# Kernel optimization log

Measured on AMD Instinct MI355X. Metric: run time of the kernel, lower is better.

## Reference

```python
import jax, jax.numpy as jnp
import numpy as np

EPS = 1e-5
HEADS, DK, DV = 8, 32, 32


def conv3x3(x, w, b):
    # regular (non-depthwise, despite the name) 3x3 conv, stride 1, padding 1
    y = jax.lax.conv_general_dilated(
        x, w, window_strides=(1, 1), padding='SAME',
        dimension_numbers=('NCHW', 'OIHW', 'NCHW'))
    return y + b[None, :, None, None]


def setup_inputs() -> dict:
    key = jax.random.key(0)
    ks = jax.random.split(key, 16)
    C = 256
    d = {}
    d['x'] = jax.random.normal(ks[0], (8, C, 32, 32), jnp.float32)
    s_lin = 1.0 / np.sqrt(C)
    s_conv = 1.0 / np.sqrt(C * 9)
    d['Wq'] = jax.random.normal(ks[1], (C, HEADS * DK), jnp.float32) * s_lin
    d['bq'] = jnp.zeros((HEADS * DK,), jnp.float32)
    d['conv_k_w'] = jax.random.normal(ks[2], (C, C, 3, 3), jnp.float32) * s_conv
    d['conv_k_b'] = jnp.zeros((C,), jnp.float32)
    d['Wk'] = jax.random.normal(ks[3], (C, HEADS * DK), jnp.float32) * s_lin
    d['bk'] = jnp.zeros((HEADS * DK,), jnp.float32)
    d['conv_v_w'] = jax.random.normal(ks[4], (C, C, 3, 3), jnp.float32) * s_conv
    d['conv_v_b'] = jnp.zeros((C,), jnp.float32)
    d['Wv'] = jax.random.normal(ks[5], (C, HEADS * DV), jnp.float32) * s_lin
    d['bv'] = jnp.zeros((HEADS * DV,), jnp.float32)
    d['Wo'] = jax.random.normal(ks[6], (HEADS * DV, C), jnp.float32) * s_lin
    d['bo'] = jnp.zeros((C,), jnp.float32)
    d['B'] = jax.random.normal(ks[7], (1, HEADS, 1024, 1024), jnp.float32) * 0.02
    return d


def reference(x, Wq, bq, conv_k_w, conv_k_b, Wk, bk, conv_v_w, conv_v_b, Wv, bv, Wo, bo, B):
    b, c, h, w = x.shape
    hw = h * w
    xr = x.reshape(b, c, hw).transpose(0, 2, 1)  # [b, hw, c]
    # F.layer_norm with normalized_shape == full shape: whole-tensor stats, no affine
    m = jnp.mean(xr)
    v = jnp.mean((xr - m) ** 2)
    xn = (xr - m) * jax.lax.rsqrt(v + EPS)

    q = (xn @ Wq + bq).reshape(b, hw, HEADS, DK).transpose(0, 2, 1, 3)  # [b,H,hw,dk]

    k = conv3x3(x, conv_k_w, conv_k_b)  # stride 1 -> same spatial size (per source)
    k = k.reshape(b, c, hw).transpose(0, 2, 1)
    k = (k @ Wk + bk).reshape(b, hw, HEADS, DK).transpose(0, 2, 1, 3)

    vv = conv3x3(x, conv_v_w, conv_v_b)
    vv = vv.reshape(b, c, hw).transpose(0, 2, 1)
    vv = (vv @ Wv + bv).reshape(b, hw, HEADS, DV).transpose(0, 2, 1, 3)

    scale = DK ** (-0.5)
    attn = jnp.einsum('bhid,bhjd->bhij', q, k) * scale + B  # [b,H,hw,hw]
    attn = jax.nn.softmax(attn, axis=-1)
    out = jnp.einsum('bhij,bhjd->bhid', attn, vv)  # [b,H,hw,dv]
    out = out.transpose(0, 2, 1, 3).reshape(b, hw, HEADS * DV)
    out = out @ Wo + bo  # [b, hw, c]
    # faithful to torch .view(b, c, h, w): raw reshape, NO transpose
    out = out.reshape(b, c, h, w)
    return out + x
```

## Files before the change

kernel.cpp:

```cpp
#include <hip/hip_runtime.h>
#include <hip/hip_bf16.h>
#include <math.h>

#define B_     8
#define C_     256
#define HW_    1024
#define NTOT   (B_*C_*HW_)
#define HEADS_ 8
#define DK_    32
#define SCALE_ 0.17677669529663687f

#define F_STATS 0
#define F_PART  16
#define F_YK2   8192
#define F_YV2   (F_YK2 + NTOT)
#define F_XB    (F_YV2 + NTOT)
#define F_WT    (F_XB + NTOT/2)
#define F_QB    (F_WT + 589824)
#define F_KB    (F_QB + NTOT/2)
#define F_VT    (F_KB + NTOT/2)

typedef float f32x4 __attribute__((ext_vector_type(4)));
typedef short short8 __attribute__((ext_vector_type(8)));

__device__ __forceinline__ short bf16s(float f) {
    __hip_bfloat16 h = __float2bfloat16(f);
    return *(short*)&h;
}
__device__ __forceinline__ unsigned pack_bf16(float a, float b) {
    unsigned ua = (unsigned short)bf16s(a);
    unsigned ub = (unsigned short)bf16s(b);
    return ua | (ub << 16);
}
__device__ __forceinline__ void gload_lds16(const short* g, short* l) {
    __builtin_amdgcn_global_load_lds(
        (const __attribute__((address_space(1))) unsigned*)g,
        (__attribute__((address_space(3))) unsigned*)l, 16, 0, 0);
}

__global__ void k_prep_x(const float* __restrict__ x, short* __restrict__ xb,
                         float* __restrict__ part) {
    __shared__ short t[64 * 258];
    __shared__ float ls[4], ls2[4];
    int b = blockIdx.x >> 4, p0 = (blockIdx.x & 15) << 6;
    int tid = threadIdx.x;
    float s = 0.f, s2 = 0.f;
    for (int i = tid; i < 256 * 64; i += 256) {
        int ci = i >> 6, p = i & 63;
        float v = x[(b * C_ + ci) * HW_ + p0 + p];
        s += v; s2 += v * v;
        t[p * 258 + ci] = bf16s(v);
    }
    for (int o = 32; o; o >>= 1) { s += __shfl_down(s, o); s2 += __shfl_down(s2, o); }
    int wid = tid >> 6, lane = tid & 63;
    if (lane == 0) { ls[wid] = s; ls2[wid] = s2; }
    __syncthreads();
    if (tid == 0) {
        float a = 0.f, bb = 0.f;
        for (int i = 0; i < 4; i++) { a += ls[i]; bb += ls2[i]; }
        part[blockIdx.x * 2] = a; part[blockIdx.x * 2 + 1] = bb;
    }
    for (int i = tid; i < 64 * 256; i += 256) {
        int p = i >> 8, ci = i & 255;
        xb[(b * HW_ + p0 + p) * C_ + ci] = t[p * 258 + ci];
    }
}

__global__ void k_stats(const float* __restrict__ part, float* __restrict__ stats) {
    __shared__ float ls[256], ls2[256];
    float s = 0.f, s2 = 0.f;
    for (int i = threadIdx.x; i < 128; i += 256) { s += part[2 * i]; s2 += part[2 * i + 1]; }
    ls[threadIdx.x] = s; ls2[threadIdx.x] = s2;
    __syncthreads();
    for (int off = 128; off; off >>= 1) {
        if (threadIdx.x < off) { ls[threadIdx.x] += ls[threadIdx.x + off]; ls2[threadIdx.x] += ls2[threadIdx.x + off]; }
        __syncthreads();
    }
    if (threadIdx.x == 0) {
        float m = ls[0] / (float)NTOT;
        float var = ls2[0] / (float)NTOT - m * m;
        stats[0] = m;
        stats[1] = rsqrtf(var + 1e-5f);
    }
}

__global__ void k_prep_w(const float* __restrict__ wk, const float* __restrict__ wv,
                         short* __restrict__ wt) {
    int idx = blockIdx.x * 256 + threadIdx.x;
    int ci0 = (idx << 2) & 255;
    int rest = idx >> 6;
    int n = rest & 511, tap = rest >> 9;
    const float* src = (n < 256) ? (wk + (n * C_) * 9) : (wv + ((n - 256) * C_) * 9);
    short4 o;
    short* op = (short*)&o;
    for (int u = 0; u < 4; u++)
        op[u] = bf16s(src[(ci0 + u) * 9 + tap]);
    *(short4*)&wt[((tap * 512 + n) * C_) + ci0] = o;
}

__global__ void k_prep_pw(const float* __restrict__ Wq, const float* __restrict__ Wk,
                          const float* __restrict__ Wv, const float* __restrict__ Wo,
                          short* __restrict__ wt4) {
    __shared__ short t[64 * 66];
    int mi = blockIdx.x >> 4, tl = blockIdx.x & 15;
    int c0 = (tl >> 2) * 64, e0 = (tl & 3) * 64;
    const float* W = mi == 0 ? Wq : mi == 1 ? Wk : mi == 2 ? Wv : Wo;
    int tid = threadIdx.x;
    for (int i = tid; i < 4096; i += 256) {
        int cl = i >> 6, el = i & 63;
        t[cl * 66 + el] = bf16s(W[(c0 + cl) * 256 + e0 + el]);
    }
    __syncthreads();
    for (int i = tid; i < 4096; i += 256) {
        int el = i >> 6, cl = i & 63;
        wt4[mi * 65536 + (e0 + el) * 256 + c0 + cl] = t[cl * 66 + el];
    }
}

__global__ void k_prep_beta(const float* __restrict__ Wq, const float* __restrict__ bq,
                            const float* __restrict__ stats, float* __restrict__ beta0) {
    __shared__ float ps[1024];
    int t = threadIdx.x, e = t & 255, part = t >> 8;
    float s = 0.f;
    for (int c = part * 64; c < part * 64 + 64; c++) s += Wq[c * 256 + e];
    ps[t] = s;
    __syncthreads();
    if (t < 256) {
        float cs = ps[t] + ps[t + 256] + ps[t + 512] + ps[t + 768];
        beta0[t] = (bq[t] - stats[0] * stats[1] * cs) * SCALE_;
    }
}

__device__ __forceinline__ int a_off(int slot, int chunk) {
    int c = chunk ^ (slot & 3);
    int s = slot ^ ((slot >> 2) & 1);
    return s * 64 + c * 16;
}

__global__ __launch_bounds__(512, 4)
void k_conv_mfma(const short* __restrict__ xb, const short* __restrict__ wt,
                 const float* __restrict__ bk, const float* __restrict__ bv,
                 float* __restrict__ yk2, float* __restrict__ yv2) {
    __shared__ short a_sh[204 * 32];
    __shared__ short b_sh[9 * 2048];
    int bid = blockIdx.x;
    int nt = bid & 7, pt = (bid >> 3) & 7, b = bid >> 6;
    int R0 = pt * 4;
    int tid = threadIdx.x;
    int w = tid >> 6, l = tid & 63;
    int wm = w >> 1, wn = w & 1;
    int col16 = l & 15, kq = l >> 4;

    int offs[2], loffs[2];
    #pragma unroll
    for (int it = 0; it < 2; it++) {
        int i = tid + it * 512;
        if (i < 816) {
            int slot = i >> 2, chunk = i & 3;
            int ty = slot / 34, tx = slot - ty * 34;
            int Y = R0 - 1 + ty, X = tx - 1;
            offs[it] = ((unsigned)Y < 32u && (unsigned)X < 32u)
                       ? ((b * HW_ + Y * 32 + X) * C_ + chunk * 8) : -1;
            loffs[it] = a_off(slot, chunk);
        } else { offs[it] = -1; loffs[it] = -1; }
    }

    int bgoff[5];
    int nbj = 0;
    #pragma unroll 1
    for (int j = w; j < 36; j += 8) {
        int S = j * 64 + l;
        int tap = S >> 8, s = S & 255;
        int colb = s >> 2, kqs = s & 3;
        int kq2 = kqs ^ ((colb >> 1) & 3);
        bgoff[nbj++] = (tap * 512 + nt * 64 + colb) * C_ + kq2 * 8;
    }

    f32x4 acc[2][2];
    #pragma unroll
    for (int m = 0; m < 2; m++)
        #pragma unroll
        for (int n = 0; n < 2; n++) acc[m][n] = (f32x4)0.f;

    int sr[2];
    #pragma unroll
    for (int nf = 0; nf < 2; nf++) {
        int colb = wn * 32 + nf * 16 + col16;
        sr[nf] = (colb << 2) | (kq ^ ((colb >> 1) & 3));
    }

    {
        short8 sv[2];
        #pragma unroll
        for (int it = 0; it < 2; it++)
            sv[it] = (offs[it] >= 0) ? *(const short8*)(xb + offs[it]) : (short8)0;
        int jj = 0;
        #pragma unroll 1
        for (int j = w; j < 36; j += 8, jj++)
            gload_lds16(wt + bgoff[jj], b_sh + j * 512);
        #pragma unroll
        for (int it = 0; it < 2; it++)
            if (loffs[it] >= 0) *(short8*)((char*)a_sh + loffs[it]) = sv[it];
    }
    __syncthreads();

    #pragma unroll 1
    for (int step = 0; step < 8; step++) {
        const char* ab = (const char*)a_sh;
        const char* bbp = (const char*)b_sh;
        #pragma unroll
        for (int tap = 0; tap < 9; tap++) {
            const int dyi = tap / 3, dxi = tap % 3;
            short8 af[2], bf[2];
            #pragma unroll
            for (int mf = 0; mf < 2; mf++) {
                int slot = (wm + dyi) * 34 + mf * 16 + col16 + dxi;
                af[mf] = *(const short8*)(ab + a_off(slot, kq));
            }
            #pragma unroll
            for (int nf = 0; nf < 2; nf++)
                bf[nf] = *(const short8*)(bbp + tap * 4096 + sr[nf] * 16);
            #pragma unroll
            for (int mf = 0; mf < 2; mf++)
                #pragma unroll
                for (int nf = 0; nf < 2; nf++)
                    acc[mf][nf] = __builtin_amdgcn_mfma_f32_16x16x32_bf16(af[mf], bf[nf], acc[mf][nf], 0, 0, 0);
        }
        if (step < 7) {
            int ci0n = step * 32 + 32;
            __syncthreads();
            short8 sv[2];
            #pragma unroll
            for (int it = 0; it < 2; it++)
                sv[it] = (offs[it] >= 0) ? *(const short8*)(xb + offs[it] + ci0n) : (short8)0;
            int jj = 0;
            #pragma unroll 1
            for (int j = w; j < 36; j += 8, jj++)
                gload_lds16(wt + bgoff[jj] + ci0n, b_sh + j * 512);
            #pragma unroll
            for (int it = 0; it < 2; it++)
                if (loffs[it] >= 0) *(short8*)((char*)a_sh + loffs[it]) = sv[it];
            __syncthreads();
        }
    }

    const bool isv = (nt >= 4);
    float* dst = isv ? yv2 : yk2;
    const float* bias = isv ? bv : bk;
    int cbase = (nt & 3) * 64 + wn * 32 + col16;
    #pragma unroll
    for (int nf = 0; nf < 2; nf++) {
        int co = cbase + nf * 16;
        float bi = bias[co];
        #pragma unroll
        for (int mf = 0; mf < 2; mf++) {
            #pragma unroll
            for (int r = 0; r < 4; r++) {
                int pixel = pt * 128 + wm * 32 + mf * 16 + kq * 4 + r;
                dst[(b * HW_ + pixel) * C_ + co] = acc[mf][nf][r] + bi;
            }
        }
    }
}

__global__ void k_proj_mfma(const short* __restrict__ xb,
                            const float* __restrict__ yk2, const float* __restrict__ yv2,
                            const short* __restrict__ wt4,
                            const float* __restrict__ bkp, const float* __restrict__ bvp,
                            const float* __restrict__ stats, const float* __restrict__ beta0,
                            short* __restrict__ qb, short* __restrict__ kb,
                            short* __restrict__ vt) {
    __shared__ char smem[17408];
    int pj = blockIdx.x, pt = blockIdx.y, b = blockIdx.z;
    int p0 = pt * 32;
    int tid = threadIdx.x, w = tid >> 6, l = tid & 63;
    int c16 = l & 15, kq = l >> 4;

    if (pj == 0) {
        #pragma unroll
        for (int it = 0; it < 4; it++) {
            int i = it * 256 + tid;
            int slab = i >> 7, rem = i & 127, slot = rem >> 2, chunk = rem & 3;
            short8 v = *(const short8*)(xb + ((b * HW_ + p0 + slot) * C_ + slab * 32 + chunk * 8));
            *(short8*)(smem + slab * 2048 + a_off(slot, chunk)) = v;
        }
    } else {
        const float* src = (pj == 1) ? yk2 : yv2;
        #pragma unroll
        for (int it = 0; it < 4; it++) {
            int i = it * 256 + tid;
            int slab = i >> 7, rem = i & 127, slot = rem >> 2, chunk = rem & 3;
            const float* sp = src + (b * HW_ + p0 + slot) * C_ + slab * 32 + chunk * 8;
            float4 f0 = *(const float4*)sp;
            float4 f1 = *(const float4*)(sp + 4);
            short8 v;
            v[0] = bf16s(f0.x); v[1] = bf16s(f0.y); v[2] = bf16s(f0.z); v[3] = bf16s(f0.w);
            v[4] = bf16s(f1.x); v[5] = bf16s(f1.y); v[6] = bf16s(f1.z); v[7] = bf16s(f1.w);
            *(short8*)(smem + slab * 2048 + a_off(slot, chunk)) = v;
        }
    }
    __syncthreads();

    const short* wt_p = wt4 + pj * 65536;
    f32x4 acc[2][4];
    #pragma unroll
    for (int m = 0; m < 2; m++)
        #pragma unroll
        for (int n = 0; n < 4; n++) acc[m][n] = (f32x4)0.f;

    for (int s = 0; s < 8; s++) {
        short8 af[2], bf[4];
        #pragma unroll
        for (int mf = 0; mf < 2; mf++)
            af[mf] = *(const short8*)(smem + s * 2048 + a_off(mf * 16 + c16, kq));
        #pragma unroll
        for (int nf = 0; nf < 4; nf++)
            bf[nf] = *(const short8*)(wt_p + (w * 64 + nf * 16 + c16) * 256 + s * 32 + kq * 8);
        #pragma unroll
        for (int mf = 0; mf < 2; mf++)
            #pragma unroll
            for (int nf = 0; nf < 4; nf++)
                acc[mf][nf] = __builtin_amdgcn_mfma_f32_16x16x32_bf16(af[mf], bf[nf], acc[mf][nf], 0, 0, 0);
    }

    float alpha = (pj == 0) ? stats[1] * SCALE_ : 1.f;
    float beta[4];
    #pragma unroll
    for (int nf = 0; nf < 4; nf++) {
        int e = w * 64 + nf * 16 + c16;
        beta[nf] = (pj == 0) ? beta0[e] : (pj == 1 ? bkp[e] : bvp[e]);
    }
    __syncthreads();

    short* rp = (short*)smem + w * 2176;
    if (pj < 2) {
        #pragma unroll
        for (int mf = 0; mf < 2; mf++)
            #pragma unroll
            for (int nf = 0; nf < 4; nf++)
                #pragma unroll
                for (int rg = 0; rg < 4; rg++) {
                    int px = mf * 16 + kq * 4 + rg, el = nf * 16 + c16;
                    rp[px * 66 + el] = bf16s(alpha * acc[mf][nf][rg] + beta[nf]);
                }
        __syncthreads();
        short* dst = (pj == 0) ? qb : kb;
        #pragma unroll
        for (int j = 0; j < 4; j++) {
            int px = j * 8 + (l >> 3), el = (l & 7) * 8;
            short8 v = *(const short8*)(rp + px * 66 + el);
            int e = w * 64 + el, h = e >> 5, d = e & 31;
            *(short8*)(dst + ((b * 8 + h) * HW_ + p0 + px) * DK_ + d) = v;
        }
    } else {
        #pragma unroll
        for (int mf = 0; mf < 2; mf++)
            #pragma unroll
            for (int nf = 0; nf < 4; nf++)
                #pragma unroll
                for (int rg = 0; rg < 4; rg++) {
                    int px = mf * 16 + kq * 4 + rg, el = nf * 16 + c16;
                    rp[el * 34 + px] = bf16s(acc[mf][nf][rg] + beta[nf]);
                }
        __syncthreads();
        #pragma unroll
        for (int j = 0; j < 4; j++) {
            int el = j * 16 + (l >> 2), px = (l & 3) * 8;
            short8 v = *(const short8*)(rp + el * 34 + px);
            int e = w * 64 + el, h = e >> 5, d = e & 31;
            *(short8*)(vt + ((b * 8 + h) * DK_ + d) * HW_ + p0 + px) = v;
        }
    }
}

__global__ __launch_bounds__(256, 4)
void k_attn(const short* __restrict__ qb, const short* __restrict__ kb,
            const short* __restrict__ vt, const float* __restrict__ Bb,
            short* __restrict__ ao) {
    __shared__ __align__(16) short Ks[128 * 32];
    __shared__ __align__(16) short Vs[32 * 128];
    int bid = blockIdx.x;
    int h = bid & 7, b = (bid >> 3) & 7, qt = bid >> 6;
    int bh = b * HEADS_ + h;
    int tid = threadIdx.x, w = tid >> 6, l = tid & 63;
    int g = l >> 4, c16 = l & 15;

    int qrow = qt * 64 + w * 16 + c16;
    short8 qf = *(const short8*)(qb + (bh * HW_ + qrow) * DK_ + g * 8);
    const float* Brow = Bb + (h * HW_ + qrow) * HW_;

    float4 breg[8];
    #pragma unroll
    for (int mt = 0; mt < 8; mt++)
        breg[mt] = *(const float4*)(Brow + mt * 16 + g * 4);

    float m_run = -1e30f, l_run = 0.f;
    f32x4 ot[2];
    ot[0] = (f32x4)0.f; ot[1] = (f32x4)0.f;

    int vrow = tid >> 4, vch = tid & 15;
    int vrow2 = (tid + 256) >> 4, vch2 = (tid + 256) & 15;
    const short* kbase = kb + bh * HW_ * DK_;

    for (int kv0 = 0; kv0 < HW_; kv0 += 128) {
        __syncthreads();
        gload_lds16(kbase + kv0 * DK_ + (w * 2) * 512 + l * 8, Ks + (w * 2) * 512);
        gload_lds16(kbase + kv0 * DK_ + (w * 2 + 1) * 512 + l * 8, Ks + (w * 2 + 1) * 512);
        {
            short8 v0 = *(const short8*)(vt + (bh * DK_ + vrow) * HW_ + kv0 + vch * 8);
            short8 v1 = *(const short8*)(vt + (bh * DK_ + vrow2) * HW_ + kv0 + vch2 * 8);
            *(short8*)((char*)Vs + vrow * 256 + ((vch * 16) ^ ((vrow & 7) << 4))) = v0;
            *(short8*)((char*)Vs + vrow2 * 256 + ((vch2 * 16) ^ ((vrow2 & 7) << 4))) = v1;
        }
        __syncthreads();

        f32x4 st[8];
        __builtin_amdgcn_s_setprio(1);
        #pragma unroll
        for (int mt = 0; mt < 8; mt++) {
            f32x4 acc;
            acc[0] = breg[mt].x; acc[1] = breg[mt].y; acc[2] = breg[mt].z; acc[3] = breg[mt].w;
            short8 kf = *(const short8*)(Ks + (mt * 16 + c16) * DK_ + g * 8);
            st[mt] = __builtin_amdgcn_mfma_f32_16x16x32_bf16(kf, qf, acc, 0, 0, 0);
        }
        __builtin_amdgcn_s_setprio(0);
        if (kv0 + 128 < HW_) {
            #pragma unroll
            for (int mt = 0; mt < 8; mt++)
                breg[mt] = *(const float4*)(Brow + kv0 + 128 + mt * 16 + g * 4);
        }

        float pmax = st[0][0];
        #pragma unroll
        for (int mt = 0; mt < 8; mt++)
            #pragma unroll
            for (int rg = 0; rg < 4; rg++) pmax = fmaxf(pmax, st[mt][rg]);
        pmax = fmaxf(pmax, __shfl_xor(pmax, 16));
        pmax = fmaxf(pmax, __shfl_xor(pmax, 32));
        if (!__all(pmax <= m_run + 8.f)) {
            float mnew = fmaxf(m_run, pmax);
            float f = __expf(m_run - mnew);
            m_run = mnew;
            l_run *= f;
            int fv = __float_as_int(f);
            #pragma unroll
            for (int rg = 0; rg < 4; rg++) {
                float fr = __int_as_float(__builtin_amdgcn_ds_bpermute((g * 4 + rg) << 2, fv));
                ot[0][rg] *= fr;
                ot[1][rg] *= fr;
            }
        }
        float s = 0.f;
        #pragma unroll
        for (int mt = 0; mt < 8; mt++)
            #pragma unroll
            for (int rg = 0; rg < 4; rg++) {
                float e_ = __expf(st[mt][rg] - m_run);
                st[mt][rg] = e_;
                s += e_;
            }
        s += __shfl_xor(s, 16);
        s += __shfl_xor(s, 32);
        l_run += s;

        short8 pa[4];
        #pragma unroll
        for (int kt = 0; kt < 4; kt++) {
            unsigned u0 = pack_bf16(st[2 * kt][0], st[2 * kt][1]);
            unsigned u1 = pack_bf16(st[2 * kt][2], st[2 * kt][3]);
            unsigned u2 = pack_bf16(st[2 * kt + 1][0], st[2 * kt + 1][1]);
            unsigned u3 = pack_bf16(st[2 * kt + 1][2], st[2 * kt + 1][3]);
            unsigned* pu = (unsigned*)&pa[kt];
            pu[0] = u0; pu[1] = u1; pu[2] = u2; pu[3] = u3;
        }

        __builtin_amdgcn_s_setprio(1);
        #pragma unroll
        for (int kt = 0; kt < 4; kt++) {
            #pragma unroll
            for (int nt = 0; nt < 2; nt++) {
                int dv = c16 + 16 * nt;
                int X0 = kt * 64 + 8 * g;
                int X1 = X0 + 32;
                int a0 = dv * 256 + ((((X0 >> 4) ^ (dv & 7)) << 4) | (X0 & 15));
                int a1 = dv * 256 + ((((X1 >> 4) ^ (dv & 7)) << 4) | (X1 & 15));
                unsigned long long lo = *(const unsigned long long*)((char*)Vs + a0);
                unsigned long long hi = *(const unsigned long long*)((char*)Vs + a1);
                short8 vf;
                *(unsigned long long*)&vf = lo;
                *((unsigned long long*)&vf + 1) = hi;
                ot[nt] = __builtin_amdgcn_mfma_f32_16x16x32_bf16(pa[kt], vf, ot[nt], 0, 0, 0);
            }
        }
        __builtin_amdgcn_s_setprio(0);
    }

    float linv = 1.f / l_run;
    int lrv = __float_as_int(linv);
    #pragma unroll
    for (int rg = 0; rg < 4; rg++) {
        float li = __int_as_float(__builtin_amdgcn_ds_bpermute((g * 4 + rg) << 2, lrv));
        int qg = qt * 64 + w * 16 + g * 4 + rg;
        #pragma unroll
        for (int nt = 0; nt < 2; nt++)
            ao[(b * HW_ + qg) * C_ + h * DK_ + nt * 16 + c16] = bf16s(ot[nt][rg] * li);
    }
}

__global__ void k_out_mfma(const short* __restrict__ aob, const short* __restrict__ wot,
                           const float* __restrict__ bo, const float* __restrict__ x,
                           float* __restrict__ out) {
    __shared__ char smem[16384];
    int pt = blockIdx.x, b = blockIdx.y;
    int p0 = pt * 32;
    int tid = threadIdx.x, w = tid >> 6, l = tid & 63;
    int c16 = l & 15, kq = l >> 4;

    #pragma unroll
    for (int it = 0; it < 4; it++) {
        int i = it * 256 + tid;
        int slab = i >> 7, rem = i & 127, slot = rem >> 2, chunk = rem & 3;
        short8 v = *(const short8*)(aob + ((b * HW_ + p0 + slot) * C_ + slab * 32 + chunk * 8));
        *(short8*)(smem + slab * 2048 + a_off(slot, chunk)) = v;
    }
    __syncthreads();

    f32x4 acc[2][4];
    #pragma unroll
    for (int m = 0; m < 2; m++)
        #pragma unroll
        for (int n = 0; n < 4; n++) acc[m][n] = (f32x4)0.f;

    for (int s = 0; s < 8; s++) {
        short8 af[2], bf[4];
        #pragma unroll
        for (int mf = 0; mf < 2; mf++)
            af[mf] = *(const short8*)(smem + s * 2048 + a_off(mf * 16 + c16, kq));
        #pragma unroll
        for (int nf = 0; nf < 4; nf++)
            bf[nf] = *(const short8*)(wot + (w * 64 + nf * 16 + c16) * 256 + s * 32 + kq * 8);
        #pragma unroll
        for (int mf = 0; mf < 2; mf++)
            #pragma unroll
            for (int nf = 0; nf < 4; nf++)
                acc[mf][nf] = __builtin_amdgcn_mfma_f32_16x16x32_bf16(af[mf], bf[nf], acc[mf][nf], 0, 0, 0);
    }

    #pragma unroll
    for (int nf = 0; nf < 4; nf++) {
        int e = w * 64 + nf * 16 + c16;
        float bov = bo[e];
        #pragma unroll
        for (int mf = 0; mf < 2; mf++) {
            #pragma unroll
            for (int rg = 0; rg < 4; rg++) {
                int px = mf * 16 + kq * 4 + rg;
                int idx = b * (C_ * HW_) + (p0 + px) * 256 + e;
                out[idx] = acc[mf][nf][rg] + bov + x[idx];
            }
        }
    }
}

extern "C" void kernel_launch(void* const* d_in, const int* in_sizes, int n_in,
                              void* d_out, int out_size, void* d_ws, size_t ws_size,
                              hipStream_t stream) {
    const float* x   = (const float*)d_in[0];
    const float* Wq  = (const float*)d_in[1];
    const float* bq  = (const float*)d_in[2];
    const float* ckw = (const float*)d_in[3];
    const float* ckb = (const float*)d_in[4];
    const float* Wk  = (const float*)d_in[5];
    const float* bk  = (const float*)d_in[6];
    const float* cvw = (const float*)d_in[7];
    const float* cvb = (const float*)d_in[8];
    const float* Wv  = (const float*)d_in[9];
    const float* bv  = (const float*)d_in[10];
    const float* Wo  = (const float*)d_in[11];
    const float* bo  = (const float*)d_in[12];
    const float* Bb  = (const float*)d_in[13];
    float* ws  = (float*)d_ws;
    float* out = (float*)d_out;

    short* xb      = (short*)(ws + F_XB);
    short* wt      = (short*)(ws + F_WT);
    short* wt4     = (short*)(ws + F_WT);
    float* beta0   = ws + F_WT + 131072;
    short* qb      = (short*)(ws + F_QB);
    short* kb      = (short*)(ws + F_KB);
    short* vt      = (short*)(ws + F_VT);
    short* aob     = (short*)(ws + F_YK2);
    short* wot     = wt4 + 3 * 65536;

    k_prep_x   <<<128,  256, 0, stream>>>(x, xb, ws + F_PART);
    k_stats    <<<1,    256, 0, stream>>>(ws + F_PART, ws + F_STATS);
    k_prep_w   <<<1152, 256, 0, stream>>>(ckw, cvw, wt);
    k_conv_mfma<<<512,  512, 0, stream>>>(xb, wt, ckb, cvb, ws + F_YK2, ws + F_YV2);
    k_prep_pw  <<<64,   256, 0, stream>>>(Wq, Wk, Wv, Wo, wt4);
    k_prep_beta<<<1,   1024, 0, stream>>>(Wq, bq, ws + F_STATS, beta0);
    k_proj_mfma<<<dim3(3, 32, 8), 256, 0, stream>>>(xb, ws + F_YK2, ws + F_YV2,
                                                    wt4, bk, bv, ws + F_STATS, beta0,
                                                    qb, kb, vt);
    k_attn     <<<1024, 256, 0, stream>>>(qb, kb, vt, Bb, aob);
    k_out_mfma <<<dim3(32, 8), 256, 0, stream>>>(aob, wot, bo, x, out);
}
```

Measured before the change: 143.1 us.

## Split attention over key halves, store conv outputs in bf16, widen prep_x grid

The attention kernel is split-K over two key halves. Each block writes unnormalized partial outputs plus running max and sum, and a new combine kernel merges them, which doubles the grid from 1024 to 2048 blocks and raises the occupancy hint. The conv kernel now writes its K/V activations as bf16 instead of fp32, so the projection kernel loads bf16 directly and moves half the bytes. k_prep_x uses 256 smaller blocks for more parallelism. The cost is an extra kernel launch and a round trip of the partial results through memory, plus an extra bf16 rounding of the partial outputs.

After: 220.6 us. 1.54x slower.

```diff
diff --git a/kernel.cpp b/kernel.cpp
--- a/kernel.cpp
+++ b/kernel.cpp
@@ -27,6 +27,10 @@
     __hip_bfloat16 h = __float2bfloat16(f);
     return *(short*)&h;
 }
+__device__ __forceinline__ float bf2f(short s) {
+    unsigned u = ((unsigned)(unsigned short)s) << 16;
+    return __int_as_float((int)u);
+}
 __device__ __forceinline__ unsigned pack_bf16(float a, float b) {
     unsigned ua = (unsigned short)bf16s(a);
     unsigned ub = (unsigned short)bf16s(b);
@@ -40,13 +44,13 @@
 
 __global__ void k_prep_x(const float* __restrict__ x, short* __restrict__ xb,
                          float* __restrict__ part) {
-    __shared__ short t[64 * 258];
+    __shared__ short t[32 * 258];
     __shared__ float ls[4], ls2[4];
-    int b = blockIdx.x >> 4, p0 = (blockIdx.x & 15) << 6;
+    int b = blockIdx.x >> 5, p0 = (blockIdx.x & 31) << 5;
     int tid = threadIdx.x;
     float s = 0.f, s2 = 0.f;
-    for (int i = tid; i < 256 * 64; i += 256) {
-        int ci = i >> 6, p = i & 63;
+    for (int i = tid; i < 256 * 32; i += 256) {
+        int ci = i >> 5, p = i & 31;
         float v = x[(b * C_ + ci) * HW_ + p0 + p];
         s += v; s2 += v * v;
         t[p * 258 + ci] = bf16s(v);
@@ -60,7 +64,7 @@
         for (int i = 0; i < 4; i++) { a += ls[i]; bb += ls2[i]; }
         part[blockIdx.x * 2] = a; part[blockIdx.x * 2 + 1] = bb;
     }
-    for (int i = tid; i < 64 * 256; i += 256) {
+    for (int i = tid; i < 32 * 256; i += 256) {
         int p = i >> 8, ci = i & 255;
         xb[(b * HW_ + p0 + p) * C_ + ci] = t[p * 258 + ci];
     }
@@ -68,8 +72,7 @@
 
 __global__ void k_stats(const float* __restrict__ part, float* __restrict__ stats) {
     __shared__ float ls[256], ls2[256];
-    float s = 0.f, s2 = 0.f;
-    for (int i = threadIdx.x; i < 128; i += 256) { s += part[2 * i]; s2 += part[2 * i + 1]; }
+    float s = part[2 * threadIdx.x], s2 = part[2 * threadIdx.x + 1];
     ls[threadIdx.x] = s; ls2[threadIdx.x] = s2;
     __syncthreads();
     for (int off = 128; off; off >>= 1) {
@@ -140,7 +143,7 @@
 __global__ __launch_bounds__(512, 4)
 void k_conv_mfma(const short* __restrict__ xb, const short* __restrict__ wt,
                  const float* __restrict__ bk, const float* __restrict__ bv,
-                 float* __restrict__ yk2, float* __restrict__ yv2) {
+                 short* __restrict__ yk2b, short* __restrict__ yv2b) {
     __shared__ short a_sh[204 * 32];
     __shared__ short b_sh[9 * 2048];
     int bid = blockIdx.x;
@@ -245,7 +248,7 @@
     }
 
     const bool isv = (nt >= 4);
-    float* dst = isv ? yv2 : yk2;
+    short* dst = isv ? yv2b : yk2b;
     const float* bias = isv ? bv : bk;
     int cbase = (nt & 3) * 64 + wn * 32 + col16;
     #pragma unroll
@@ -257,14 +260,14 @@
             #pragma unroll
             for (int r = 0; r < 4; r++) {
                 int pixel = pt * 128 + wm * 32 + mf * 16 + kq * 4 + r;
-                dst[(b * HW_ + pixel) * C_ + co] = acc[mf][nf][r] + bi;
+                dst[(b * HW_ + pixel) * C_ + co] = bf16s(acc[mf][nf][r] + bi);
             }
         }
     }
 }
 
 __global__ void k_proj_mfma(const short* __restrict__ xb,
-                            const float* __restrict__ yk2, const float* __restrict__ yv2,
+                            const short* __restrict__ yk2b, const short* __restrict__ yv2b,
                             const short* __restrict__ wt4,
                             const float* __restrict__ bkp, const float* __restrict__ bvp,
                             const float* __restrict__ stats, const float* __restrict__ beta0,
@@ -276,28 +279,13 @@
     int tid = threadIdx.x, w = tid >> 6, l = tid & 63;
     int c16 = l & 15, kq = l >> 4;
 
-    if (pj == 0) {
-        #pragma unroll
-        for (int it = 0; it < 4; it++) {
-            int i = it * 256 + tid;
-            int slab = i >> 7, rem = i & 127, slot = rem >> 2, chunk = rem & 3;
-            short8 v = *(const short8*)(xb + ((b * HW_ + p0 + slot) * C_ + slab * 32 + chunk * 8));
-            *(short8*)(smem + slab * 2048 + a_off(slot, chunk)) = v;
-        }
-    } else {
-        const float* src = (pj == 1) ? yk2 : yv2;
-        #pragma unroll
-        for (int it = 0; it < 4; it++) {
-            int i = it * 256 + tid;
-            int slab = i >> 7, rem = i & 127, slot = rem >> 2, chunk = rem & 3;
-            const float* sp = src + (b * HW_ + p0 + slot) * C_ + slab * 32 + chunk * 8;
-            float4 f0 = *(const float4*)sp;
-            float4 f1 = *(const float4*)(sp + 4);
-            short8 v;
-            v[0] = bf16s(f0.x); v[1] = bf16s(f0.y); v[2] = bf16s(f0.z); v[3] = bf16s(f0.w);
-            v[4] = bf16s(f1.x); v[5] = bf16s(f1.y); v[6] = bf16s(f1.z); v[7] = bf16s(f1.w);
-            *(short8*)(smem + slab * 2048 + a_off(slot, chunk)) = v;
-        }
+    const short* src = pj == 0 ? xb : (pj == 1 ? yk2b : yv2b);
+    #pragma unroll
+    for (int it = 0; it < 4; it++) {
+        int i = it * 256 + tid;
+        int slab = i >> 7, rem = i & 127, slot = rem >> 2, chunk = rem & 3;
+        short8 v = *(const short8*)(src + ((b * HW_ + p0 + slot) * C_ + slab * 32 + chunk * 8));
+        *(short8*)(smem + slab * 2048 + a_off(slot, chunk)) = v;
     }
     __syncthreads();
 
@@ -373,14 +361,14 @@
     }
 }
 
-__global__ __launch_bounds__(256, 4)
+__global__ __launch_bounds__(256, 8)
 void k_attn(const short* __restrict__ qb, const short* __restrict__ kb,
             const short* __restrict__ vt, const float* __restrict__ Bb,
-            short* __restrict__ ao) {
+            short* __restrict__ pob, float* __restrict__ pml) {
     __shared__ __align__(16) short Ks[128 * 32];
     __shared__ __align__(16) short Vs[32 * 128];
     int bid = blockIdx.x;
-    int h = bid & 7, b = (bid >> 3) & 7, qt = bid >> 6;
+    int h = bid & 7, b = (bid >> 3) & 7, qt = (bid >> 6) & 15, ks = bid >> 10;
     int bh = b * HEADS_ + h;
     int tid = threadIdx.x, w = tid >> 6, l = tid & 63;
     int g = l >> 4, c16 = l & 15;
@@ -388,11 +376,12 @@
     int qrow = qt * 64 + w * 16 + c16;
     short8 qf = *(const short8*)(qb + (bh * HW_ + qrow) * DK_ + g * 8);
     const float* Brow = Bb + (h * HW_ + qrow) * HW_;
+    const int kbeg = ks * 512, kend = kbeg + 512;
 
     float4 breg[8];
     #pragma unroll
     for (int mt = 0; mt < 8; mt++)
-        breg[mt] = *(const float4*)(Brow + mt * 16 + g * 4);
+        breg[mt] = *(const float4*)(Brow + kbeg + mt * 16 + g * 4);
 
     float m_run = -1e30f, l_run = 0.f;
     f32x4 ot[2];
@@ -402,7 +391,7 @@
     int vrow2 = (tid + 256) >> 4, vch2 = (tid + 256) & 15;
     const short* kbase = kb + bh * HW_ * DK_;
 
-    for (int kv0 = 0; kv0 < HW_; kv0 += 128) {
+    for (int kv0 = kbeg; kv0 < kend; kv0 += 128) {
         __syncthreads();
         gload_lds16(kbase + kv0 * DK_ + (w * 2) * 512 + l * 8, Ks + (w * 2) * 512);
         gload_lds16(kbase + kv0 * DK_ + (w * 2 + 1) * 512 + l * 8, Ks + (w * 2 + 1) * 512);
@@ -424,7 +413,7 @@
             st[mt] = __builtin_amdgcn_mfma_f32_16x16x32_bf16(kf, qf, acc, 0, 0, 0);
         }
         __builtin_amdgcn_s_setprio(0);
-        if (kv0 + 128 < HW_) {
+        if (kv0 + 128 < kend) {
             #pragma unroll
             for (int mt = 0; mt < 8; mt++)
                 breg[mt] = *(const float4*)(Brow + kv0 + 128 + mt * 16 + g * 4);
@@ -495,16 +484,39 @@
         __builtin_amdgcn_s_setprio(0);
     }
 
-    float linv = 1.f / l_run;
-    int lrv = __float_as_int(linv);
+    int rowbase = (ks << 16) + (bh << 10);
+    if (g == 0)
+        *(float2*)(pml + 2 * (rowbase + qrow)) = make_float2(m_run, l_run);
     #pragma unroll
     for (int rg = 0; rg < 4; rg++) {
-        float li = __int_as_float(__builtin_amdgcn_ds_bpermute((g * 4 + rg) << 2, lrv));
-        int qg = qt * 64 + w * 16 + g * 4 + rg;
+        int row = rowbase + qt * 64 + w * 16 + g * 4 + rg;
         #pragma unroll
         for (int nt = 0; nt < 2; nt++)
-            ao[(b * HW_ + qg) * C_ + h * DK_ + nt * 16 + c16] = bf16s(ot[nt][rg] * li);
-    }
+            pob[row * 32 + c16 + 16 * nt] = bf16s(ot[nt][rg]);
+    }
+}
+
+__global__ void k_comb(const short* __restrict__ pob, const float* __restrict__ pml,
+                       short* __restrict__ aob) {
+    int idx = blockIdx.x * 256 + threadIdx.x;
+    int row = idx >> 3, dq = (idx & 7) * 4;
+    float2 ml1 = *(const float2*)(pml + 2 * row);
+    float2 ml2 = *(const float2*)(pml + 2 * (65536 + row));
+    float mstar = fmaxf(ml1.x, ml2.x);
+    float w1 = __expf(ml1.x - mstar), w2 = __expf(ml2.x - mstar);
+    float dinv = 1.f / (w1 * ml1.y + w2 * ml2.y);
+    short4 o1 = *(const short4*)&pob[row * 32 + dq];
+    short4 o2 = *(const short4*)&pob[2097152 + row * 32 + dq];
+    int b = row >> 13, h = (row >> 10) & 7, qg = row & 1023;
+    short* dst = aob + (b * HW_ + qg) * C_ + h * DK_ + dq;
+    short* o1p = (short*)&o1;
+    short* o2p = (short*)&o2;
+    short4 r;
+    short* rp = (short*)&r;
+    #pragma unroll
+    for (int j = 0; j < 4; j++)
+        rp[j] = bf16s((w1 * bf2f(o1p[j]) + w2 * bf2f(o2p[j])) * dinv);
+    *(short4*)dst = r;
 }
 
 __global__ void k_out_mfma(const short* __restrict__ aob, const short* __restrict__ wot,
@@ -589,18 +601,23 @@
     short* qb      = (short*)(ws + F_QB);
     short* kb      = (short*)(ws + F_KB);
     short* vt      = (short*)(ws + F_VT);
+    short* yk2b    = (short*)(ws + F_YK2);
+    short* yv2b    = (short*)(ws + F_YV2);
     short* aob     = (short*)(ws + F_YK2);
+    short* pob     = (short*)(ws + F_YV2);
+    float* pml     = ws + F_XB;
     short* wot     = wt4 + 3 * 65536;
 
-    k_prep_x   <<<128,  256, 0, stream>>>(x, xb, ws + F_PART);
+    k_prep_x   <<<256,  256, 0, stream>>>(x, xb, ws + F_PART);
     k_stats    <<<1,    256, 0, stream>>>(ws + F_PART, ws + F_STATS);
     k_prep_w   <<<1152, 256, 0, stream>>>(ckw, cvw, wt);
-    k_conv_mfma<<<512,  512, 0, stream>>>(xb, wt, ckb, cvb, ws + F_YK2, ws + F_YV2);
+    k_conv_mfma<<<512,  512, 0, stream>>>(xb, wt, ckb, cvb, yk2b, yv2b);
     k_prep_pw  <<<64,   256, 0, stream>>>(Wq, Wk, Wv, Wo, wt4);
     k_prep_beta<<<1,   1024, 0, stream>>>(Wq, bq, ws + F_STATS, beta0);
-    k_proj_mfma<<<dim3(3, 32, 8), 256, 0, stream>>>(xb, ws + F_YK2, ws + F_YV2,
+    k_proj_mfma<<<dim3(3, 32, 8), 256, 0, stream>>>(xb, yk2b, yv2b,
                                                     wt4, bk, bv, ws + F_STATS, beta0,
                                                     qb, kb, vt);
-    k_attn     <<<1024, 256, 0, stream>>>(qb, kb, vt, Bb, aob);
+    k_attn     <<<2048, 256, 0, stream>>>(qb, kb, vt, Bb, pob, pml);
+    k_comb     <<<2048, 256, 0, stream>>>(pob, pml, aob);
     k_out_mfma <<<dim3(32, 8), 256, 0, stream>>>(aob, wot, bo, x, out);
 }
```

## Store conv outputs as bf16 and split prep_x into smaller blocks

Applied to the files above, without the earlier changes.

The conv kernel now writes its K and V intermediates as bf16 instead of fp32, and the projection kernel loads them directly as short8 without converting. This halves the write traffic of the conv and the read traffic of the projection. The x-prep kernel also uses 256 blocks of 32 pixels instead of 128 blocks of 64, and k_stats is adjusted to read 256 partials. Rounding is unchanged because the values were already converted to bf16 before the MFMA.

Result: faster. 131.5 us (-8.1%).

```diff
diff --git a/kernel.cpp b/kernel.cpp
--- a/kernel.cpp
+++ b/kernel.cpp
@@ -40,13 +40,13 @@
 
 __global__ void k_prep_x(const float* __restrict__ x, short* __restrict__ xb,
                          float* __restrict__ part) {
-    __shared__ short t[64 * 258];
+    __shared__ short t[32 * 258];
     __shared__ float ls[4], ls2[4];
-    int b = blockIdx.x >> 4, p0 = (blockIdx.x & 15) << 6;
+    int b = blockIdx.x >> 5, p0 = (blockIdx.x & 31) << 5;
     int tid = threadIdx.x;
     float s = 0.f, s2 = 0.f;
-    for (int i = tid; i < 256 * 64; i += 256) {
-        int ci = i >> 6, p = i & 63;
+    for (int i = tid; i < 256 * 32; i += 256) {
+        int ci = i >> 5, p = i & 31;
         float v = x[(b * C_ + ci) * HW_ + p0 + p];
         s += v; s2 += v * v;
         t[p * 258 + ci] = bf16s(v);
@@ -60,7 +60,7 @@
         for (int i = 0; i < 4; i++) { a += ls[i]; bb += ls2[i]; }
         part[blockIdx.x * 2] = a; part[blockIdx.x * 2 + 1] = bb;
     }
-    for (int i = tid; i < 64 * 256; i += 256) {
+    for (int i = tid; i < 32 * 256; i += 256) {
         int p = i >> 8, ci = i & 255;
         xb[(b * HW_ + p0 + p) * C_ + ci] = t[p * 258 + ci];
     }
@@ -68,8 +68,7 @@
 
 __global__ void k_stats(const float* __restrict__ part, float* __restrict__ stats) {
     __shared__ float ls[256], ls2[256];
-    float s = 0.f, s2 = 0.f;
-    for (int i = threadIdx.x; i < 128; i += 256) { s += part[2 * i]; s2 += part[2 * i + 1]; }
+    float s = part[2 * threadIdx.x], s2 = part[2 * threadIdx.x + 1];
     ls[threadIdx.x] = s; ls2[threadIdx.x] = s2;
     __syncthreads();
     for (int off = 128; off; off >>= 1) {
@@ -140,7 +139,7 @@
 __global__ __launch_bounds__(512, 4)
 void k_conv_mfma(const short* __restrict__ xb, const short* __restrict__ wt,
                  const float* __restrict__ bk, const float* __restrict__ bv,
-                 float* __restrict__ yk2, float* __restrict__ yv2) {
+                 short* __restrict__ yk2b, short* __restrict__ yv2b) {
     __shared__ short a_sh[204 * 32];
     __shared__ short b_sh[9 * 2048];
     int bid = blockIdx.x;
@@ -245,7 +244,7 @@
     }
 
     const bool isv = (nt >= 4);
-    float* dst = isv ? yv2 : yk2;
+    short* dst = isv ? yv2b : yk2b;
     const float* bias = isv ? bv : bk;
     int cbase = (nt & 3) * 64 + wn * 32 + col16;
     #pragma unroll
@@ -257,14 +256,14 @@
             #pragma unroll
             for (int r = 0; r < 4; r++) {
                 int pixel = pt * 128 + wm * 32 + mf * 16 + kq * 4 + r;
-                dst[(b * HW_ + pixel) * C_ + co] = acc[mf][nf][r] + bi;
+                dst[(b * HW_ + pixel) * C_ + co] = bf16s(acc[mf][nf][r] + bi);
             }
         }
     }
 }
 
 __global__ void k_proj_mfma(const short* __restrict__ xb,
-                            const float* __restrict__ yk2, const float* __restrict__ yv2,
+                            const short* __restrict__ yk2b, const short* __restrict__ yv2b,
                             const short* __restrict__ wt4,
                             const float* __restrict__ bkp, const float* __restrict__ bvp,
                             const float* __restrict__ stats, const float* __restrict__ beta0,
@@ -276,28 +275,13 @@
     int tid = threadIdx.x, w = tid >> 6, l = tid & 63;
     int c16 = l & 15, kq = l >> 4;
 
-    if (pj == 0) {
-        #pragma unroll
-        for (int it = 0; it < 4; it++) {
-            int i = it * 256 + tid;
-            int slab = i >> 7, rem = i & 127, slot = rem >> 2, chunk = rem & 3;
-            short8 v = *(const short8*)(xb + ((b * HW_ + p0 + slot) * C_ + slab * 32 + chunk * 8));
-            *(short8*)(smem + slab * 2048 + a_off(slot, chunk)) = v;
-        }
-    } else {
-        const float* src = (pj == 1) ? yk2 : yv2;
-        #pragma unroll
-        for (int it = 0; it < 4; it++) {
-            int i = it * 256 + tid;
-            int slab = i >> 7, rem = i & 127, slot = rem >> 2, chunk = rem & 3;
-            const float* sp = src + (b * HW_ + p0 + slot) * C_ + slab * 32 + chunk * 8;
-            float4 f0 = *(const float4*)sp;
-            float4 f1 = *(const float4*)(sp + 4);
-            short8 v;
-            v[0] = bf16s(f0.x); v[1] = bf16s(f0.y); v[2] = bf16s(f0.z); v[3] = bf16s(f0.w);
-            v[4] = bf16s(f1.x); v[5] = bf16s(f1.y); v[6] = bf16s(f1.z); v[7] = bf16s(f1.w);
-            *(short8*)(smem + slab * 2048 + a_off(slot, chunk)) = v;
-        }
+    const short* src = pj == 0 ? xb : (pj == 1 ? yk2b : yv2b);
+    #pragma unroll
+    for (int it = 0; it < 4; it++) {
+        int i = it * 256 + tid;
+        int slab = i >> 7, rem = i & 127, slot = rem >> 2, chunk = rem & 3;
+        short8 v = *(const short8*)(src + ((b * HW_ + p0 + slot) * C_ + slab * 32 + chunk * 8));
+        *(short8*)(smem + slab * 2048 + a_off(slot, chunk)) = v;
     }
     __syncthreads();
 
@@ -589,16 +573,18 @@
     short* qb      = (short*)(ws + F_QB);
     short* kb      = (short*)(ws + F_KB);
     short* vt      = (short*)(ws + F_VT);
+    short* yk2b    = (short*)(ws + F_YK2);
+    short* yv2b    = (short*)(ws + F_YV2);
     short* aob     = (short*)(ws + F_YK2);
     short* wot     = wt4 + 3 * 65536;
 
-    k_prep_x   <<<128,  256, 0, stream>>>(x, xb, ws + F_PART);
+    k_prep_x   <<<256,  256, 0, stream>>>(x, xb, ws + F_PART);
     k_stats    <<<1,    256, 0, stream>>>(ws + F_PART, ws + F_STATS);
     k_prep_w   <<<1152, 256, 0, stream>>>(ckw, cvw, wt);
-    k_conv_mfma<<<512,  512, 0, stream>>>(xb, wt, ckb, cvb, ws + F_YK2, ws + F_YV2);
+    k_conv_mfma<<<512,  512, 0, stream>>>(xb, wt, ckb, cvb, yk2b, yv2b);
     k_prep_pw  <<<64,   256, 0, stream>>>(Wq, Wk, Wv, Wo, wt4);
     k_prep_beta<<<1,   1024, 0, stream>>>(Wq, bq, ws + F_STATS, beta0);
-    k_proj_mfma<<<dim3(3, 32, 8), 256, 0, stream>>>(xb, ws + F_YK2, ws + F_YV2,
+    k_proj_mfma<<<dim3(3, 32, 8), 256, 0, stream>>>(xb, yk2b, yv2b,
                                                     wt4, bk, bv, ws + F_STATS, beta0,
                                                     qb, kb, vt);
     k_attn     <<<1024, 256, 0, stream>>>(qb, kb, vt, Bb, aob);
```
